# Optimization experiments

Measured on AMD Instinct MI355X. Metric: run time of the kernel, lower is better.

Reference implementation:

```python
import jax, jax.numpy as jnp
import numpy as np

N, C, E, G = 100000, 200, 400000, 512
H, D = 4, 50  # heads, per-head dim (out_channels // num_heads)
NEG_SLOPE = 0.2
EPS_LN = 1e-5


def setup_inputs() -> dict:
    key = jax.random.key(0)
    ks = jax.random.split(key, 12)
    x = jax.random.normal(ks[0], (N, C), dtype=jnp.float32)
    edge_index = jax.random.randint(ks[1], (2, E), 0, N, dtype=jnp.int64)
    batch = jnp.sort(jax.random.randint(ks[2], (N,), 0, G, dtype=jnp.int64))
    # LayerNorm (graph mode) affine params
    ln_w = jnp.ones((C,), jnp.float32)
    ln_b = jnp.zeros((C,), jnp.float32)
    # GATConv params: W [C, H*D], att_src/att_dst [H, D], bias [H*D]
    s = 1.0 / np.sqrt(C)
    W_gat = jax.random.uniform(ks[3], (C, H * D), jnp.float32, -s, s)
    att_src = jax.random.uniform(ks[4], (H, D), jnp.float32, -s, s)
    att_dst = jax.random.uniform(ks[5], (H, D), jnp.float32, -s, s)
    bias_gat = jnp.zeros((H * D,), jnp.float32)
    # SAGPooling scoring GraphConv(C -> 1): lin_rel (with bias) + lin_root (no bias)
    w_rel = jax.random.uniform(ks[6], (C, 1), jnp.float32, -s, s)
    b_rel = jnp.zeros((1,), jnp.float32)
    w_root = jax.random.uniform(ks[7], (C, 1), jnp.float32, -s, s)
    return {"x": x, "edge_index": edge_index, "batch": batch,
            "ln_w": ln_w, "ln_b": ln_b, "W_gat": W_gat, "att_src": att_src,
            "att_dst": att_dst, "bias_gat": bias_gat,
            "w_rel": w_rel, "b_rel": b_rel, "w_root": w_root}


def reference(x, edge_index, batch, ln_w, ln_b, W_gat, att_src, att_dst,
              bias_gat, w_rel, b_rel, w_root):
    n = x.shape[0]
    # --- PyG LayerNorm, mode='graph': normalize over all nodes+channels per graph
    cnt = jax.ops.segment_sum(jnp.ones((n,), x.dtype), batch, G)          # [G]
    denom = cnt * C
    mean = jax.ops.segment_sum(x.sum(-1), batch, G) / denom               # [G]
    ex2 = jax.ops.segment_sum((x * x).sum(-1), batch, G) / denom          # [G]
    var = ex2 - mean * mean
    h = (x - mean[batch, None]) * jax.lax.rsqrt(var + EPS_LN)[batch, None]
    h = h * ln_w + ln_b
    h = jax.nn.elu(h)
    # --- GATConv (concat heads, self-loops added, eval-mode dropout)
    loops = jnp.arange(n, dtype=edge_index.dtype)
    src = jnp.concatenate([edge_index[0], loops])                          # [E+N]
    dst = jnp.concatenate([edge_index[1], loops])
    xh = (h @ W_gat).reshape(n, H, D)                                      # [N,H,D]
    a_src = (xh * att_src).sum(-1)                                         # [N,H]
    a_dst = (xh * att_dst).sum(-1)
    alpha = jax.nn.leaky_relu(a_src[src] + a_dst[dst], NEG_SLOPE)          # [E+N,H]
    m = jax.ops.segment_max(alpha, dst, n)                                 # segment softmax
    e = jnp.exp(alpha - m[dst])
    z = jax.ops.segment_sum(e, dst, n)
    att = e / (z[dst] + 1e-16)
    out = jax.ops.segment_sum(xh[src] * att[:, :, None], dst, n)           # [N,H,D]
    out = out.reshape(n, H * D) + bias_gat                                 # [N,C]
    # --- SAGPooling(min_score=-1): GraphConv score -> per-graph softmax -> multiply
    agg = jax.ops.segment_sum(out[edge_index[0]], edge_index[1], n)        # neighbor sum
    score = (agg @ w_rel + b_rel + out @ w_root)[:, 0]                     # [N]
    sm = score - jax.ops.segment_max(score, batch, G)[batch]
    es = jnp.exp(sm)
    score = es / jax.ops.segment_sum(es, batch, G)[batch]
    # softmax scores in (0,1) > min_score=-1 -> all nodes kept, x scaled by score
    xp = out * score[:, None]                                              # [N,C]
    # --- global_add_pool
    g = jax.ops.segment_sum(xp, batch, G)                                  # [G,C]
    return (xp, g)
```

## Files before the change

### kernel.cpp

```cpp
#include <hip/hip_runtime.h>
#include <hip/hip_bf16.h>

#define NN 100000
#define CC 200
#define EE 400000
#define GG 512

typedef __bf16 bf16x8 __attribute__((ext_vector_type(8)));
typedef float f32x4 __attribute__((ext_vector_type(4)));

__device__ __forceinline__ float bfraw(unsigned int u) { return __uint_as_float(u << 16); }
__device__ __forceinline__ unsigned short f2bfraw(float f) {
  __hip_bfloat16 b = __float2bfloat16(f);
  union { __hip_bfloat16 b; unsigned short u; } cv; cv.b = b; return cv.u;
}

__global__ void k_detect(const unsigned int* __restrict__ lnw_raw,
                         const unsigned int* __restrict__ ei_raw, int* __restrict__ flags) {
  if (threadIdx.x == 0 && blockIdx.x == 0) {
    flags[0] = (lnw_raw[0] == 0x3F800000u) ? 1 : 0;
    flags[1] = (ei_raw[1] == 0u && ei_raw[3] == 0u && ei_raw[5] == 0u && ei_raw[7] == 0u) ? 1 : 0;
  }
}

__global__ void k_cvt_idx(const int* __restrict__ raw, const int* __restrict__ flags,
                          int* __restrict__ out, int count) {
  int i = blockIdx.x * 256 + threadIdx.x;
  if (i >= count) return;
  out[i] = flags[1] ? raw[2 * i] : raw[i];
}

__global__ void k_cvt_params(const void* lnw, const void* lnb, const void* W,
                             const void* attS, const void* attD, const void* bias,
                             const void* wrel, const void* brel, const void* wroot,
                             const int* __restrict__ flags, unsigned short* __restrict__ out) {
  int i = blockIdx.x * 256 + threadIdx.x;
  if (i > 41400) return;
  const void* p; int off;
  if (i < 200)        { p = lnw;  off = i; }
  else if (i < 400)   { p = lnb;  off = i - 200; }
  else if (i < 40400) { p = W;    off = i - 400; }
  else if (i < 40600) { p = attS; off = i - 40400; }
  else if (i < 40800) { p = attD; off = i - 40600; }
  else if (i < 41000) { p = bias; off = i - 40800; }
  else if (i < 41200) { p = wrel; off = i - 41000; }
  else if (i < 41400) { p = wroot; off = i - 41200; }
  else                { p = brel; off = 0; }
  out[i] = flags[0] ? f2bfraw(((const float*)p)[off]) : ((const unsigned short*)p)[off];
}

__global__ void k_starts(const int* __restrict__ batch, int* __restrict__ starts) {
  int i = blockIdx.x * 256 + threadIdx.x;
  if (i >= NN) return;
  int b = batch[i];
  int pb = (i == 0) ? -1 : batch[i - 1];
  for (int g = pb + 1; g <= b; ++g) starts[g] = i;
  if (i == NN - 1) {
    for (int g = b + 1; g <= GG; ++g) starts[g] = NN;
  }
}

__global__ void k_ln_stats(const void* __restrict__ x, const int* __restrict__ starts,
                           const int* __restrict__ flags, float* __restrict__ gacc) {
  __shared__ float sh1[4], sh2[4];
  int g = blockIdx.x >> 3, chunk = blockIdx.x & 7;
  int r0 = starts[g], r1 = starts[g + 1], cnt = r1 - r0;
  int ra = r0 + (cnt * chunk) / 8;
  int rb = r0 + (cnt * (chunk + 1)) / 8;
  float s1 = 0.f, s2 = 0.f;
  if (flags[0]) {
    const float4* xv = (const float4*)x;
    for (int i = ra * 50 + (int)threadIdx.x; i < rb * 50; i += 256) {
      float4 r = xv[i];
      s1 += r.x + r.y + r.z + r.w;
      s2 += r.x * r.x + r.y * r.y + r.z * r.z + r.w * r.w;
    }
  } else {
    const uint4* xv = (const uint4*)x;
    for (int i = ra * 25 + (int)threadIdx.x; i < rb * 25; i += 256) {
      uint4 r = xv[i];
      unsigned int w[4] = {r.x, r.y, r.z, r.w};
#pragma unroll
      for (int j = 0; j < 4; ++j) {
        float a = bfraw(w[j] & 0xffffu);
        float b = bfraw(w[j] >> 16);
        s1 += a + b; s2 += a * a + b * b;
      }
    }
  }
#pragma unroll
  for (int o = 32; o > 0; o >>= 1) { s1 += __shfl_down(s1, o, 64); s2 += __shfl_down(s2, o, 64); }
  if ((threadIdx.x & 63) == 0) { sh1[threadIdx.x >> 6] = s1; sh2[threadIdx.x >> 6] = s2; }
  __syncthreads();
  if (threadIdx.x == 0) {
    atomicAdd(&gacc[g * 2],     sh1[0] + sh1[1] + sh1[2] + sh1[3]);
    atomicAdd(&gacc[g * 2 + 1], sh2[0] + sh2[1] + sh2[2] + sh2[3]);
  }
}

__global__ void k_ln_fin(const float* __restrict__ gacc, const int* __restrict__ starts,
                         float* __restrict__ mean, float* __restrict__ rstd) {
  int g = blockIdx.x * 64 + threadIdx.x;
  if (g >= GG) return;
  int cnt = starts[g + 1] - starts[g];
  if (cnt > 0) {
    float denom = (float)cnt * (float)CC;
    float m = gacc[g * 2] / denom;
    float var = gacc[g * 2 + 1] / denom - m * m;
    mean[g] = m;
    rstd[g] = rsqrtf(var + 1e-5f);
  } else { mean[g] = 0.f; rstd[g] = 0.f; }
}

__global__ void k_norm(const void* __restrict__ x, const int* __restrict__ batch,
                       const float* __restrict__ mean, const float* __restrict__ rstd,
                       const unsigned short* __restrict__ lnw, const unsigned short* __restrict__ lnb,
                       const int* __restrict__ flags, unsigned short* __restrict__ h) {
  int gi = blockIdx.x * 256 + threadIdx.x;
  if (gi >= NN * 25) return;
  int row = gi / 25, sub = gi - row * 25;
  int b = batch[row];
  float m = mean[b], rs = rstd[b];
  int cbase = sub * 8;
  float v[8];
  if (flags[0]) {
    const float* xf = (const float*)x + row * CC + cbase;
    float4 r0 = *(const float4*)xf, r1 = *(const float4*)(xf + 4);
    v[0]=r0.x; v[1]=r0.y; v[2]=r0.z; v[3]=r0.w; v[4]=r1.x; v[5]=r1.y; v[6]=r1.z; v[7]=r1.w;
  } else {
    uint4 r = *(const uint4*)((const unsigned short*)x + row * CC + cbase);
    unsigned int w[4] = {r.x, r.y, r.z, r.w};
#pragma unroll
    for (int j = 0; j < 4; ++j) { v[2*j] = bfraw(w[j] & 0xffffu); v[2*j+1] = bfraw(w[j] >> 16); }
  }
  unsigned int o[4];
#pragma unroll
  for (int j = 0; j < 4; ++j) {
    int c0 = cbase + 2 * j;
    float ta = (v[2*j]   - m) * rs * bfraw(lnw[c0])     + bfraw(lnb[c0]);
    float tb = (v[2*j+1] - m) * rs * bfraw(lnw[c0 + 1]) + bfraw(lnb[c0 + 1]);
    ta = ta > 0.f ? ta : expm1f(ta);
    tb = tb > 0.f ? tb : expm1f(tb);
    o[j] = (unsigned int)f2bfraw(ta) | ((unsigned int)f2bfraw(tb) << 16);
  }
  *(uint4*)(h + row * CC + cbase) = make_uint4(o[0], o[1], o[2], o[3]);
}

__global__ void k_wpack(const unsigned short* __restrict__ W, unsigned short* __restrict__ wp) {
  int idx = blockIdx.x * 256 + threadIdx.x;
  if (idx >= 13 * 7 * 64 * 8) return;
  int j = idx & 7;
  int rest = idx >> 3;
  int l = rest & 63;
  int ts = rest >> 6;
  int s = ts % 7, t = ts / 7;
  int k = s * 32 + (l >> 4) * 8 + j;
  int n = t * 16 + (l & 15);
  wp[idx] = (k < CC && n < CC) ? W[k * CC + n] : (unsigned short)0;
}

__global__ void k_gemm(const unsigned short* __restrict__ h, const unsigned short* __restrict__ wp,
                       unsigned short* __restrict__ xh) {
  int gw = (blockIdx.x * 256 + threadIdx.x) >> 6;
  int lane = threadIdx.x & 63;
  int mbase = gw * 16;
  if (mbase >= NN) return;
  int quad = lane >> 4, l15 = lane & 15;
  f32x4 acc[13];
#pragma unroll
  for (int t = 0; t < 13; ++t) { f32x4 z = {0.f, 0.f, 0.f, 0.f}; acc[t] = z; }
  const unsigned short* hrow = h + (mbase + l15) * CC + quad * 8;
  const bf16x8* wv = (const bf16x8*)wp;
#pragma unroll
  for (int s = 0; s < 7; ++s) {
    bf16x8 af = *(const bf16x8*)(hrow + s * 32);
#pragma unroll
    for (int t = 0; t < 13; ++t) {
      bf16x8 bf = wv[(t * 7 + s) * 64 + lane];
      acc[t] = __builtin_amdgcn_mfma_f32_16x16x32_bf16(af, bf, acc[t], 0, 0, 0);
    }
  }
#pragma unroll
  for (int t = 0; t < 13; ++t) {
    int c = t * 16 + l15;
    if (c < CC) {
#pragma unroll
      for (int r = 0; r < 4; ++r) {
        int mrow = mbase + quad * 4 + r;
        xh[mrow * CC + c] = f2bfraw(acc[t][r]);
      }
    }
  }
}

__global__ void k_attdots(const unsigned short* __restrict__ xh, const unsigned short* __restrict__ attS,
                          const unsigned short* __restrict__ attD,
                          float* __restrict__ asrc, float* __restrict__ adst) {
  int idx = blockIdx.x * 256 + threadIdx.x;
  if (idx >= NN * 4) return;
  int n = idx >> 2, hh = idx & 3;
  const unsigned int* row = (const unsigned int*)(xh + n * CC + hh * 50);
  const unsigned int* ws  = (const unsigned int*)(attS + hh * 50);
  const unsigned int* wd  = (const unsigned int*)(attD + hh * 50);
  float s = 0.f, d = 0.f;
#pragma unroll
  for (int i = 0; i < 25; ++i) {
    unsigned int rv = row[i], sv = ws[i], dv = wd[i];
    float a0 = bfraw(rv & 0xffffu), a1 = bfraw(rv >> 16);
    s += a0 * bfraw(sv & 0xffffu) + a1 * bfraw(sv >> 16);
    d += a0 * bfraw(dv & 0xffffu) + a1 * bfraw(dv >> 16);
  }
  asrc[idx] = s; adst[idx] = d;
}

__global__ void k_hist(const int* __restrict__ ei32, int* __restrict__ deg) {
  int e = blockIdx.x * 256 + threadIdx.x;
  if (e >= EE) return;
  atomicAdd(&deg[ei32[EE + e]], 1);
}

__global__ void k_scan1(const int* __restrict__ deg, int* __restrict__ rowptr, int* __restrict__ sums) {
  __shared__ int sh[256];
  int tid = threadIdx.x;
  int base = blockIdx.x * 1024 + tid * 4;
  int v[4]; int s = 0;
#pragma unroll
  for (int j = 0; j < 4; ++j) { int i = base + j; v[j] = (i < NN) ? deg[i] : 0; s += v[j]; }
  sh[tid] = s;
  __syncthreads();
  for (int o = 1; o < 256; o <<= 1) {
    int t = (tid >= o) ? sh[tid - o] : 0;
    __syncthreads();
    sh[tid] += t;
    __syncthreads();
  }
  int run = sh[tid] - s;
#pragma unroll
  for (int j = 0; j < 4; ++j) { int i = base + j; if (i < NN) rowptr[i] = run; run += v[j]; }
  if (tid == 255) sums[blockIdx.x] = sh[255];
}

__global__ void k_scan2(int* __restrict__ sums, int nb) {
  if (blockIdx.x == 0 && threadIdx.x == 0) {
    int run = 0;
    for (int i = 0; i < nb; ++i) { int t = sums[i]; sums[i] = run; run += t; }
  }
}

__global__ void k_scan3(int* __restrict__ rowptr, const int* __restrict__ sums) {
  int tid = threadIdx.x;
  int add = sums[blockIdx.x];
  int base = blockIdx.x * 1024 + tid * 4;
#pragma unroll
  for (int j = 0; j < 4; ++j) { int i = base + j; if (i < NN) rowptr[i] += add; }
  if (blockIdx.x == 0 && tid == 0) rowptr[NN] = EE;
}

__global__ void k_scatter(const int* __restrict__ ei32, const int* __restrict__ rowptr,
                          int* __restrict__ fill, int* __restrict__ csrc) {
  int e = blockIdx.x * 256 + threadIdx.x;
  if (e >= EE) return;
  int s = ei32[e], d = ei32[EE + e];
  int pos = rowptr[d] + atomicAdd(&fill[d], 1);
  csrc[pos] = s;
}

__global__ void k_attn_z(const float* __restrict__ asrc, const float* __restrict__ adst,
                         const int* __restrict__ rowptr, const int* __restrict__ csrc,
                         float* __restrict__ att, float* __restrict__ z, float* __restrict__ eself) {
  int n = blockIdx.x * 256 + threadIdx.x;
  if (n >= NN) return;
  float4 ad4 = *(const float4*)(adst + n * 4);
  float4 as4 = *(const float4*)(asrc + n * 4);
  float ade[4] = {ad4.x, ad4.y, ad4.z, ad4.w};
  float ase[4] = {as4.x, as4.y, as4.z, as4.w};
  float zz[4], es[4];
#pragma unroll
  for (int hh = 0; hh < 4; ++hh) {
    float al = ase[hh] + ade[hh];
    al = al > 0.f ? al : 0.2f * al;
    es[hh] = __expf(al); zz[hh] = es[hh];
  }
  *(float4*)(eself + n * 4) = make_float4(es[0], es[1], es[2], es[3]);
  int p0 = rowptr[n], p1 = rowptr[n + 1];
  for (int p = p0; p < p1; ++p) {
    int s = csrc[p];
    float4 av = *(const float4*)(asrc + s * 4);
    float a4[4] = {av.x, av.y, av.z, av.w}, e4[4];
#pragma unroll
    for (int hh = 0; hh < 4; ++hh) {
      float al = a4[hh] + ade[hh];
      al = al > 0.f ? al : 0.2f * al;
      e4[hh] = __expf(al);
      zz[hh] += e4[hh];
    }
    *(float4*)(att + p * 4) = make_float4(e4[0], e4[1], e4[2], e4[3]);
  }
  *(float4*)(z + n * 4) = make_float4(zz[0], zz[1], zz[2], zz[3]);
}

__global__ void k_out(const unsigned short* __restrict__ xh, const float* __restrict__ att,
                      const float* __restrict__ z, const float* __restrict__ eself,
                      const int* __restrict__ rowptr, const int* __restrict__ csrc,
                      const unsigned short* __restrict__ bias, const unsigned short* __restrict__ wrel,
                      const unsigned short* __restrict__ wroot,
                      unsigned short* __restrict__ out,
                      float* __restrict__ srel, float* __restrict__ sroot) {
  __shared__ float sA[256], sB[256];
  int tid = threadIdx.x;
  int local = tid / 25;
  int sub = tid - local * 25;
  int n = blockIdx.x * 10 + local;
  bool active = (local < 10) && (n < NN);
  float pr = 0.f, pq = 0.f;
  if (active) {
    int c0 = sub * 8;
    int hh0 = c0 / 50;
    int hh1 = hh0 < 3 ? hh0 + 1 : hh0;
    int bnd = (hh0 + 1) * 50;
    bool cr[8];
#pragma unroll
    for (int j = 0; j < 8; ++j) cr[j] = (c0 + j) >= bnd;
    float e_lo = eself[n * 4 + hh0], e_hi = eself[n * 4 + hh1];
    float rz_lo = 1.f / (z[n * 4 + hh0] + 1e-16f);
    float rz_hi = 1.f / (z[n * 4 + hh1] + 1e-16f);
    float acc[8];
    uint4 xv = *(const uint4*)(xh + (size_t)n * CC + c0);
    {
      unsigned int w[4] = {xv.x, xv.y, xv.z, xv.w};
#pragma unroll
      for (int j = 0; j < 4; ++j) {
        float lo = bfraw(w[j] & 0xffffu), hi = bfraw(w[j] >> 16);
        acc[2*j]   = (cr[2*j]   ? e_hi : e_lo) * lo;
        acc[2*j+1] = (cr[2*j+1] ? e_hi : e_lo) * hi;
      }
    }
    int p0 = rowptr[n], p1 = rowptr[n + 1];
    for (int p = p0; p < p1; ++p) {
      int s = csrc[p];
      float a_lo = att[p * 4 + hh0];
      float a_hi = att[p * 4 + hh1];
      uint4 gv = *(const uint4*)(xh + (size_t)s * CC + c0);
      unsigned int gw[4] = {gv.x, gv.y, gv.z, gv.w};
#pragma unroll
      for (int j = 0; j < 4; ++j) {
        float lo = bfraw(gw[j] & 0xffffu), hi = bfraw(gw[j] >> 16);
        acc[2*j]   += (cr[2*j]   ? a_hi : a_lo) * lo;
        acc[2*j+1] += (cr[2*j+1] ? a_hi : a_lo) * hi;
      }
    }
    uint4 bv = *(const uint4*)(bias + c0);
    uint4 rv = *(const uint4*)(wrel + c0);
    uint4 qv = *(const uint4*)(wroot + c0);
    unsigned int bw[4] = {bv.x, bv.y, bv.z, bv.w};
    unsigned int rw[4] = {rv.x, rv.y, rv.z, rv.w};
    unsigned int qw[4] = {qv.x, qv.y, qv.z, qv.w};
    unsigned int ow[4];
#pragma unroll
    for (int j = 0; j < 4; ++j) {
      float v0 = acc[2*j]   * (cr[2*j]   ? rz_hi : rz_lo) + bfraw(bw[j] & 0xffffu);
      float v1 = acc[2*j+1] * (cr[2*j+1] ? rz_hi : rz_lo) + bfraw(bw[j] >> 16);
      ow[j] = (unsigned int)f2bfraw(v0) | ((unsigned int)f2bfraw(v1) << 16);
      pr += v0 * bfraw(rw[j] & 0xffffu) + v1 * bfraw(rw[j] >> 16);
      pq += v0 * bfraw(qw[j] & 0xffffu) + v1 * bfraw(qw[j] >> 16);
    }
    *(uint4*)(out + (size_t)n * CC + c0) = make_uint4(ow[0], ow[1], ow[2], ow[3]);
  }
  sA[tid] = pr; sB[tid] = pq;
  __syncthreads();
  if (active && sub == 0) {
    float a = 0.f, b = 0.f;
#pragma unroll
    for (int k = 0; k < 25; ++k) { a += sA[tid + k]; b += sB[tid + k]; }
    srel[n] = a; sroot[n] = b;
  }
}

__global__ void k_score(const float* __restrict__ srel, const float* __restrict__ sroot,
                        const unsigned short* __restrict__ brel, const int* __restrict__ rowptr,
                        const int* __restrict__ csrc, float* __restrict__ score) {
  int n = blockIdx.x * 256 + threadIdx.x;
  if (n >= NN) return;
  float sc = bfraw(brel[0]) + sroot[n];
  int p0 = rowptr[n], p1 = rowptr[n + 1];
  for (int p = p0; p < p1; ++p) sc += srel[csrc[p]];
  score[n] = sc;
}

__global__ void k_gsoftmax(const float* __restrict__ score, const int* __restrict__ starts,
                           float* __restrict__ smax, float* __restrict__ ssum) {
  __shared__ float sh[4];
  __shared__ float bc;
  int g = blockIdx.x;
  int r0 = starts[g], r1 = starts[g + 1];
  float m = -3.0e38f;
  for (int i = r0 + (int)threadIdx.x; i < r1; i += 256) m = fmaxf(m, score[i]);
#pragma unroll
  for (int o = 32; o > 0; o >>= 1) m = fmaxf(m, __shfl_down(m, o, 64));
  if ((threadIdx.x & 63) == 0) sh[threadIdx.x >> 6] = m;
  __syncthreads();
  if (threadIdx.x == 0) bc = fmaxf(fmaxf(sh[0], sh[1]), fmaxf(sh[2], sh[3]));
  __syncthreads();
  float mm = bc;
  float s = 0.f;
  for (int i = r0 + (int)threadIdx.x; i < r1; i += 256) s += expf(score[i] - mm);
#pragma unroll
  for (int o = 32; o > 0; o >>= 1) s += __shfl_down(s, o, 64);
  if ((threadIdx.x & 63) == 0) sh[threadIdx.x >> 6] = s;
  __syncthreads();
  if (threadIdx.x == 0) { smax[g] = mm; ssum[g] = sh[0] + sh[1] + sh[2] + sh[3]; }
}

__global__ void k_scoref(const float* __restrict__ score, const int* __restrict__ batch,
                         const float* __restrict__ smax, const float* __restrict__ ssum,
                         float* __restrict__ scoref) {
  int n = blockIdx.x * 256 + threadIdx.x;
  if (n >= NN) return;
  int b = batch[n];
  float d = ssum[b];
  scoref[n] = (d > 0.f) ? expf(score[n] - smax[b]) / d : 0.f;
}

__global__ void k_xp(const unsigned short* __restrict__ out, const float* __restrict__ scoref,
                     const int* __restrict__ flags, void* __restrict__ dout) {
  int gi = blockIdx.x * 256 + threadIdx.x;
  if (gi >= NN * 25) return;
  int r = gi / 25, sub = gi - r * 25;
  float sf = scoref[r];
  uint4 xv = *(const uint4*)(out + (size_t)r * CC + sub * 8);
  unsigned int w[4] = {xv.x, xv.y, xv.z, xv.w};
  if (flags[0]) {
    float v[8];
#pragma unroll
    for (int j = 0; j < 4; ++j) { v[2*j] = bfraw(w[j] & 0xffffu) * sf; v[2*j+1] = bfraw(w[j] >> 16) * sf; }
    float* dp = (float*)dout + (size_t)r * CC + sub * 8;
    *(float4*)dp       = make_float4(v[0], v[1], v[2], v[3]);
    *(float4*)(dp + 4) = make_float4(v[4], v[5], v[6], v[7]);
  } else {
    unsigned int o[4];
#pragma unroll
    for (int j = 0; j < 4; ++j) {
      float lo = bfraw(w[j] & 0xffffu) * sf, hi = bfraw(w[j] >> 16) * sf;
      o[j] = (unsigned int)f2bfraw(lo) | ((unsigned int)f2bfraw(hi) << 16);
    }
    *(uint4*)((unsigned short*)dout + (size_t)r * CC + sub * 8) = make_uint4(o[0], o[1], o[2], o[3]);
  }
}

__global__ void k_gsum(const unsigned short* __restrict__ out, const float* __restrict__ scoref,
                       const int* __restrict__ starts, const int* __restrict__ flags,
                       void* __restrict__ dout) {
  __shared__ float part[10][200];
  int tid = threadIdx.x;
  int rg = tid / 25, sub = tid - rg * 25;
  int g = blockIdx.x;
  int r0 = starts[g], r1 = starts[g + 1];
  if (rg < 10) {
    float acc[8];
#pragma unroll
    for (int j = 0; j < 8; ++j) acc[j] = 0.f;
    for (int r = r0 + rg; r < r1; r += 10) {
      float sf = scoref[r];
      uint4 xv = *(const uint4*)(out + (size_t)r * CC + sub * 8);
      unsigned int w[4] = {xv.x, xv.y, xv.z, xv.w};
#pragma unroll
      for (int j = 0; j < 4; ++j) {
        acc[2*j]   += bfraw(w[j] & 0xffffu) * sf;
        acc[2*j+1] += bfraw(w[j] >> 16) * sf;
      }
    }
#pragma unroll
    for (int j = 0; j < 8; ++j) part[rg][sub * 8 + j] = acc[j];
  }
  __syncthreads();
  if (tid < 200) {
    float s = 0.f;
#pragma unroll
    for (int k = 0; k < 10; ++k) s += part[k][tid];
    size_t o = (size_t)NN * CC + (size_t)g * CC + tid;
    if (flags[0]) ((float*)dout)[o] = s;
    else ((unsigned short*)dout)[o] = f2bfraw(s);
  }
}

constexpr size_t O_FLAGS  = 0;
constexpr size_t O_STARTS = 16;
constexpr size_t O_MEAN   = 2080;
constexpr size_t O_RSTD   = 4128;
constexpr size_t O_SMAX   = 6176;
constexpr size_t O_SSUM   = 8224;
constexpr size_t O_SUMS   = 10272;
constexpr size_t O_PAR    = 10784;
constexpr size_t O_WPACK  = 93600;
constexpr size_t O_BATCH  = 186784;
constexpr size_t O_EI32   = 586784;
constexpr size_t O_DEG    = 3786784;
constexpr size_t O_FILL   = 4186784;
constexpr size_t O_ROWPTR = 4586784;
constexpr size_t O_CSRC   = 4986912;
constexpr size_t O_ASRC   = 6586912;
constexpr size_t O_ADST   = 8186912;
constexpr size_t O_SREL   = 9786912;
constexpr size_t O_SROOT  = 10186912;
constexpr size_t O_SCORE  = 10586912;
constexpr size_t O_SCOREF = 10986912;
constexpr size_t O_Z      = 11386912;
constexpr size_t O_ESELF  = 12986912;
constexpr size_t O_ATT    = 14586912;
constexpr size_t O_XH     = 20986912;
constexpr size_t O_OUT    = 60986912;

extern "C" void kernel_launch(void* const* d_in, const int* in_sizes, int n_in,
                              void* d_out, int out_size, void* d_ws, size_t ws_size,
                              hipStream_t stream) {
  const void* x     = d_in[0];
  const int*  ei    = (const int*)d_in[1];
  const int*  batchr= (const int*)d_in[2];
  const void* lnw_r = d_in[3];
  const void* lnb_r = d_in[4];
  const void* Wg_r  = d_in[5];
  const void* attS_r= d_in[6];
  const void* attD_r= d_in[7];
  const void* bias_r= d_in[8];
  const void* wrel_r= d_in[9];
  const void* brel_r= d_in[10];
  const void* wroot_r=d_in[11];

  char* ws = (char*)d_ws;
  int*   flags  = (int*)(ws + O_FLAGS);
  int*   starts = (int*)(ws + O_STARTS);
  float* mean   = (float*)(ws + O_MEAN);
  float* rstd   = (float*)(ws + O_RSTD);
  float* smax   = (float*)(ws + O_SMAX);
  float* ssum   = (float*)(ws + O_SSUM);
  int*   sums   = (int*)(ws + O_SUMS);
  unsigned short* par = (unsigned short*)(ws + O_PAR);
  unsigned short* wpack = (unsigned short*)(ws + O_WPACK);
  int*   batch  = (int*)(ws + O_BATCH);
  int*   ei32   = (int*)(ws + O_EI32);
  int*   deg    = (int*)(ws + O_DEG);
  int*   fill   = (int*)(ws + O_FILL);
  int*   rowptr = (int*)(ws + O_ROWPTR);
  int*   csrc   = (int*)(ws + O_CSRC);
  float* asrc   = (float*)(ws + O_ASRC);
  float* adst   = (float*)(ws + O_ADST);
  float* srel   = (float*)(ws + O_SREL);
  float* sroot  = (float*)(ws + O_SROOT);
  float* score  = (float*)(ws + O_SCORE);
  float* scoref = (float*)(ws + O_SCOREF);
  float* z      = (float*)(ws + O_Z);
  float* eself  = (float*)(ws + O_ESELF);
  float* att    = (float*)(ws + O_ATT);
  float* gacc   = (float*)(ws + O_ATT);
  unsigned short* xh    = (unsigned short*)(ws + O_XH);
  unsigned short* outws = (unsigned short*)(ws + O_OUT);

  unsigned short* lnw  = par;
  unsigned short* lnb  = par + 200;
  unsigned short* Wc   = par + 400;
  unsigned short* attS = par + 40400;
  unsigned short* attD = par + 40600;
  unsigned short* bias = par + 40800;
  unsigned short* wrel = par + 41000;
  unsigned short* wroot= par + 41200;
  unsigned short* brel = par + 41400;

  unsigned short* h = (unsigned short*)d_out;

  hipMemsetAsync(deg, 0, 800000, stream);
  hipMemsetAsync(gacc, 0, 4096, stream);

  k_detect    <<<1, 64, 0, stream>>>((const unsigned int*)lnw_r, (const unsigned int*)ei, flags);
  k_cvt_params<<<162, 256, 0, stream>>>(lnw_r, lnb_r, Wg_r, attS_r, attD_r, bias_r,
                                        wrel_r, brel_r, wroot_r, flags, par);
  k_cvt_idx   <<<(2 * EE + 255) / 256, 256, 0, stream>>>(ei, flags, ei32, 2 * EE);
  k_cvt_idx   <<<(NN + 255) / 256, 256, 0, stream>>>(batchr, flags, batch, NN);
  k_starts    <<<(NN + 255) / 256, 256, 0, stream>>>(batch, starts);
  k_ln_stats  <<<GG * 8, 256, 0, stream>>>(x, starts, flags, gacc);
  k_ln_fin    <<<8, 64, 0, stream>>>(gacc, starts, mean, rstd);
  k_norm      <<<(NN * 25 + 255) / 256, 256, 0, stream>>>(x, batch, mean, rstd, lnw, lnb, flags, h);
  k_wpack     <<<(13 * 7 * 64 * 8 + 255) / 256, 256, 0, stream>>>(Wc, wpack);
  k_gemm      <<<1563, 256, 0, stream>>>(h, wpack, xh);
  k_attdots   <<<(NN * 4 + 255) / 256, 256, 0, stream>>>(xh, attS, attD, asrc, adst);
  k_hist      <<<(EE + 255) / 256, 256, 0, stream>>>(ei32, deg);
  k_scan1     <<<98, 256, 0, stream>>>(deg, rowptr, sums);
  k_scan2     <<<1, 64, 0, stream>>>(sums, 98);
  k_scan3     <<<98, 256, 0, stream>>>(rowptr, sums);
  k_scatter   <<<(EE + 255) / 256, 256, 0, stream>>>(ei32, rowptr, fill, csrc);
  k_attn_z    <<<(NN + 255) / 256, 256, 0, stream>>>(asrc, adst, rowptr, csrc, att, z, eself);
  k_out       <<<10000, 256, 0, stream>>>(xh, att, z, eself, rowptr, csrc, bias, wrel, wroot,
                                          outws, srel, sroot);
  k_score     <<<(NN + 255) / 256, 256, 0, stream>>>(srel, sroot, brel, rowptr, csrc, score);
  k_gsoftmax  <<<GG, 256, 0, stream>>>(score, starts, smax, ssum);
  k_scoref    <<<(NN + 255) / 256, 256, 0, stream>>>(score, batch, smax, ssum, scoref);
  k_xp        <<<(NN * 25 + 255) / 256, 256, 0, stream>>>(outws, scoref, flags, d_out);
  k_gsum      <<<GG, 256, 0, stream>>>(outws, scoref, starts, flags, d_out);
}
```

Before: 415.6 us.

## Fuse layernorm into GEMM, histogram into edge conversion, and xp with pooling

Layer-norm and ELU are now applied while loading GEMM A fragments, eliminating the intermediate normalized buffer. The degree histogram is folded into edge index conversion, and the block-sum scan becomes a parallel shared-memory scan. The gather loops in the attention-output and score kernels are unrolled by two for more memory-level parallelism. Output scaling and global add pooling are merged into one pass split across 8 chunks per graph, using atomics and a final conversion kernel.

```diff
diff --git a/kernel.cpp b/kernel.cpp
--- a/kernel.cpp
+++ b/kernel.cpp
@@ -28,6 +28,15 @@
   int i = blockIdx.x * 256 + threadIdx.x;
   if (i >= count) return;
   out[i] = flags[1] ? raw[2 * i] : raw[i];
+}
+
+__global__ void k_cvt_edges(const int* __restrict__ raw, const int* __restrict__ flags,
+                            int* __restrict__ out, int* __restrict__ deg) {
+  int i = blockIdx.x * 256 + threadIdx.x;
+  if (i >= 2 * EE) return;
+  int v = flags[1] ? raw[2 * i] : raw[i];
+  out[i] = v;
+  if (i >= EE) atomicAdd(&deg[v], 1);
 }
 
 __global__ void k_cvt_params(const void* lnw, const void* lnb, const void* W,
@@ -112,40 +121,6 @@
   } else { mean[g] = 0.f; rstd[g] = 0.f; }
 }
 
-__global__ void k_norm(const void* __restrict__ x, const int* __restrict__ batch,
-                       const float* __restrict__ mean, const float* __restrict__ rstd,
-                       const unsigned short* __restrict__ lnw, const unsigned short* __restrict__ lnb,
-                       const int* __restrict__ flags, unsigned short* __restrict__ h) {
-  int gi = blockIdx.x * 256 + threadIdx.x;
-  if (gi >= NN * 25) return;
-  int row = gi / 25, sub = gi - row * 25;
-  int b = batch[row];
-  float m = mean[b], rs = rstd[b];
-  int cbase = sub * 8;
-  float v[8];
-  if (flags[0]) {
-    const float* xf = (const float*)x + row * CC + cbase;
-    float4 r0 = *(const float4*)xf, r1 = *(const float4*)(xf + 4);
-    v[0]=r0.x; v[1]=r0.y; v[2]=r0.z; v[3]=r0.w; v[4]=r1.x; v[5]=r1.y; v[6]=r1.z; v[7]=r1.w;
-  } else {
-    uint4 r = *(const uint4*)((const unsigned short*)x + row * CC + cbase);
-    unsigned int w[4] = {r.x, r.y, r.z, r.w};
-#pragma unroll
-    for (int j = 0; j < 4; ++j) { v[2*j] = bfraw(w[j] & 0xffffu); v[2*j+1] = bfraw(w[j] >> 16); }
-  }
-  unsigned int o[4];
-#pragma unroll
-  for (int j = 0; j < 4; ++j) {
-    int c0 = cbase + 2 * j;
-    float ta = (v[2*j]   - m) * rs * bfraw(lnw[c0])     + bfraw(lnb[c0]);
-    float tb = (v[2*j+1] - m) * rs * bfraw(lnw[c0 + 1]) + bfraw(lnb[c0 + 1]);
-    ta = ta > 0.f ? ta : expm1f(ta);
-    tb = tb > 0.f ? tb : expm1f(tb);
-    o[j] = (unsigned int)f2bfraw(ta) | ((unsigned int)f2bfraw(tb) << 16);
-  }
-  *(uint4*)(h + row * CC + cbase) = make_uint4(o[0], o[1], o[2], o[3]);
-}
-
 __global__ void k_wpack(const unsigned short* __restrict__ W, unsigned short* __restrict__ wp) {
   int idx = blockIdx.x * 256 + threadIdx.x;
   if (idx >= 13 * 7 * 64 * 8) return;
@@ -159,25 +134,61 @@
   wp[idx] = (k < CC && n < CC) ? W[k * CC + n] : (unsigned short)0;
 }
 
-__global__ void k_gemm(const unsigned short* __restrict__ h, const unsigned short* __restrict__ wp,
-                       unsigned short* __restrict__ xh) {
+__global__ void k_ngemm(const void* __restrict__ x, const int* __restrict__ batch,
+                        const float* __restrict__ mean, const float* __restrict__ rstd,
+                        const unsigned short* __restrict__ lnw, const unsigned short* __restrict__ lnb,
+                        const unsigned short* __restrict__ wp, const int* __restrict__ flags,
+                        unsigned short* __restrict__ xh) {
   int gw = (blockIdx.x * 256 + threadIdx.x) >> 6;
   int lane = threadIdx.x & 63;
   int mbase = gw * 16;
   if (mbase >= NN) return;
   int quad = lane >> 4, l15 = lane & 15;
+  int row = mbase + l15;
+  int b = batch[row];
+  float m = mean[b], rs = rstd[b];
+  bool f32in = flags[0] != 0;
   f32x4 acc[13];
 #pragma unroll
-  for (int t = 0; t < 13; ++t) { f32x4 z = {0.f, 0.f, 0.f, 0.f}; acc[t] = z; }
-  const unsigned short* hrow = h + (mbase + l15) * CC + quad * 8;
+  for (int t = 0; t < 13; ++t) { f32x4 zz = {0.f, 0.f, 0.f, 0.f}; acc[t] = zz; }
   const bf16x8* wv = (const bf16x8*)wp;
 #pragma unroll
   for (int s = 0; s < 7; ++s) {
-    bf16x8 af = *(const bf16x8*)(hrow + s * 32);
+    int kb = s * 32 + quad * 8;
+    union { bf16x8 v; unsigned short u[8]; unsigned int w[4]; } af;
+    if (kb < CC) {
+      float v[8];
+      if (f32in) {
+        const float* xp = (const float*)x + (size_t)row * CC + kb;
+        float4 a = *(const float4*)xp, c = *(const float4*)(xp + 4);
+        v[0]=a.x; v[1]=a.y; v[2]=a.z; v[3]=a.w; v[4]=c.x; v[5]=c.y; v[6]=c.z; v[7]=c.w;
+      } else {
+        uint4 r = *(const uint4*)((const unsigned short*)x + (size_t)row * CC + kb);
+        unsigned int w[4] = {r.x, r.y, r.z, r.w};
+#pragma unroll
+        for (int j = 0; j < 4; ++j) { v[2*j] = bfraw(w[j] & 0xffffu); v[2*j+1] = bfraw(w[j] >> 16); }
+      }
+      uint4 wv4 = *(const uint4*)(lnw + kb);
+      uint4 bv4 = *(const uint4*)(lnb + kb);
+      unsigned int ww[4] = {wv4.x, wv4.y, wv4.z, wv4.w};
+      unsigned int bb[4] = {bv4.x, bv4.y, bv4.z, bv4.w};
+#pragma unroll
+      for (int j = 0; j < 4; ++j) {
+        float t0 = (v[2*j]   - m) * rs * bfraw(ww[j] & 0xffffu) + bfraw(bb[j] & 0xffffu);
+        float t1 = (v[2*j+1] - m) * rs * bfraw(ww[j] >> 16)     + bfraw(bb[j] >> 16);
+        t0 = t0 > 0.f ? t0 : __expf(t0) - 1.f;
+        t1 = t1 > 0.f ? t1 : __expf(t1) - 1.f;
+        af.u[2*j]   = f2bfraw(t0);
+        af.u[2*j+1] = f2bfraw(t1);
+      }
+    } else {
+#pragma unroll
+      for (int j = 0; j < 4; ++j) af.w[j] = 0u;
+    }
 #pragma unroll
     for (int t = 0; t < 13; ++t) {
       bf16x8 bf = wv[(t * 7 + s) * 64 + lane];
-      acc[t] = __builtin_amdgcn_mfma_f32_16x16x32_bf16(af, bf, acc[t], 0, 0, 0);
+      acc[t] = __builtin_amdgcn_mfma_f32_16x16x32_bf16(af.v, bf, acc[t], 0, 0, 0);
     }
   }
 #pragma unroll
@@ -187,7 +198,7 @@
 #pragma unroll
       for (int r = 0; r < 4; ++r) {
         int mrow = mbase + quad * 4 + r;
-        xh[mrow * CC + c] = f2bfraw(acc[t][r]);
+        xh[(size_t)mrow * CC + c] = f2bfraw(acc[t][r]);
       }
     }
   }
@@ -199,7 +210,7 @@
   int idx = blockIdx.x * 256 + threadIdx.x;
   if (idx >= NN * 4) return;
   int n = idx >> 2, hh = idx & 3;
-  const unsigned int* row = (const unsigned int*)(xh + n * CC + hh * 50);
+  const unsigned int* row = (const unsigned int*)(xh + (size_t)n * CC + hh * 50);
   const unsigned int* ws  = (const unsigned int*)(attS + hh * 50);
   const unsigned int* wd  = (const unsigned int*)(attD + hh * 50);
   float s = 0.f, d = 0.f;
@@ -213,12 +224,6 @@
   asrc[idx] = s; adst[idx] = d;
 }
 
-__global__ void k_hist(const int* __restrict__ ei32, int* __restrict__ deg) {
-  int e = blockIdx.x * 256 + threadIdx.x;
-  if (e >= EE) return;
-  atomicAdd(&deg[ei32[EE + e]], 1);
-}
-
 __global__ void k_scan1(const int* __restrict__ deg, int* __restrict__ rowptr, int* __restrict__ sums) {
   __shared__ int sh[256];
   int tid = threadIdx.x;
@@ -241,10 +246,18 @@
 }
 
 __global__ void k_scan2(int* __restrict__ sums, int nb) {
-  if (blockIdx.x == 0 && threadIdx.x == 0) {
-    int run = 0;
-    for (int i = 0; i < nb; ++i) { int t = sums[i]; sums[i] = run; run += t; }
-  }
+  __shared__ int sh[128];
+  int tid = threadIdx.x;
+  int v = (tid < nb) ? sums[tid] : 0;
+  sh[tid] = v;
+  __syncthreads();
+  for (int o = 1; o < 128; o <<= 1) {
+    int t = (tid >= o) ? sh[tid - o] : 0;
+    __syncthreads();
+    sh[tid] += t;
+    __syncthreads();
+  }
+  if (tid < nb) sums[tid] = sh[tid] - v;
 }
 
 __global__ void k_scan3(int* __restrict__ rowptr, const int* __restrict__ sums) {
@@ -270,8 +283,8 @@
                          float* __restrict__ att, float* __restrict__ z, float* __restrict__ eself) {
   int n = blockIdx.x * 256 + threadIdx.x;
   if (n >= NN) return;
-  float4 ad4 = *(const float4*)(adst + n * 4);
-  float4 as4 = *(const float4*)(asrc + n * 4);
+  float4 ad4 = *(const float4*)(adst + (size_t)n * 4);
+  float4 as4 = *(const float4*)(asrc + (size_t)n * 4);
   float ade[4] = {ad4.x, ad4.y, ad4.z, ad4.w};
   float ase[4] = {as4.x, as4.y, as4.z, as4.w};
   float zz[4], es[4];
@@ -281,11 +294,11 @@
     al = al > 0.f ? al : 0.2f * al;
     es[hh] = __expf(al); zz[hh] = es[hh];
   }
-  *(float4*)(eself + n * 4) = make_float4(es[0], es[1], es[2], es[3]);
+  *(float4*)(eself + (size_t)n * 4) = make_float4(es[0], es[1], es[2], es[3]);
   int p0 = rowptr[n], p1 = rowptr[n + 1];
   for (int p = p0; p < p1; ++p) {
     int s = csrc[p];
-    float4 av = *(const float4*)(asrc + s * 4);
+    float4 av = *(const float4*)(asrc + (size_t)s * 4);
     float a4[4] = {av.x, av.y, av.z, av.w}, e4[4];
 #pragma unroll
     for (int hh = 0; hh < 4; ++hh) {
@@ -294,9 +307,9 @@
       e4[hh] = __expf(al);
       zz[hh] += e4[hh];
     }
-    *(float4*)(att + p * 4) = make_float4(e4[0], e4[1], e4[2], e4[3]);
-  }
-  *(float4*)(z + n * 4) = make_float4(zz[0], zz[1], zz[2], zz[3]);
+    *(float4*)(att + (size_t)p * 4) = make_float4(e4[0], e4[1], e4[2], e4[3]);
+  }
+  *(float4*)(z + (size_t)n * 4) = make_float4(zz[0], zz[1], zz[2], zz[3]);
 }
 
 __global__ void k_out(const unsigned short* __restrict__ xh, const float* __restrict__ att,
@@ -325,8 +338,8 @@
     float rz_lo = 1.f / (z[n * 4 + hh0] + 1e-16f);
     float rz_hi = 1.f / (z[n * 4 + hh1] + 1e-16f);
     float acc[8];
-    uint4 xv = *(const uint4*)(xh + (size_t)n * CC + c0);
     {
+      uint4 xv = *(const uint4*)(xh + (size_t)n * CC + c0);
       unsigned int w[4] = {xv.x, xv.y, xv.z, xv.w};
 #pragma unroll
       for (int j = 0; j < 4; ++j) {
@@ -336,17 +349,41 @@
       }
     }
     int p0 = rowptr[n], p1 = rowptr[n + 1];
-    for (int p = p0; p < p1; ++p) {
-      int s = csrc[p];
-      float a_lo = att[p * 4 + hh0];
-      float a_hi = att[p * 4 + hh1];
-      uint4 gv = *(const uint4*)(xh + (size_t)s * CC + c0);
-      unsigned int gw[4] = {gv.x, gv.y, gv.z, gv.w};
+    int p = p0;
+    for (; p + 2 <= p1; p += 2) {
+      int s0 = csrc[p], s1 = csrc[p + 1];
+      uint4 g0 = *(const uint4*)(xh + (size_t)s0 * CC + c0);
+      uint4 g1 = *(const uint4*)(xh + (size_t)s1 * CC + c0);
+      float4 av0 = *(const float4*)(att + (size_t)p * 4);
+      float4 av1 = *(const float4*)(att + (size_t)(p + 1) * 4);
+      float a0lo = hh0 == 0 ? av0.x : hh0 == 1 ? av0.y : hh0 == 2 ? av0.z : av0.w;
+      float a0hi = hh1 == 1 ? av0.y : hh1 == 2 ? av0.z : av0.w;
+      float a1lo = hh0 == 0 ? av1.x : hh0 == 1 ? av1.y : hh0 == 2 ? av1.z : av1.w;
+      float a1hi = hh1 == 1 ? av1.y : hh1 == 2 ? av1.z : av1.w;
+      unsigned int w0[4] = {g0.x, g0.y, g0.z, g0.w};
+      unsigned int w1[4] = {g1.x, g1.y, g1.z, g1.w};
 #pragma unroll
       for (int j = 0; j < 4; ++j) {
-        float lo = bfraw(gw[j] & 0xffffu), hi = bfraw(gw[j] >> 16);
-        acc[2*j]   += (cr[2*j]   ? a_hi : a_lo) * lo;
-        acc[2*j+1] += (cr[2*j+1] ? a_hi : a_lo) * hi;
+        acc[2*j]   += (cr[2*j]   ? a0hi : a0lo) * bfraw(w0[j] & 0xffffu);
+        acc[2*j+1] += (cr[2*j+1] ? a0hi : a0lo) * bfraw(w0[j] >> 16);
+      }
+#pragma unroll
+      for (int j = 0; j < 4; ++j) {
+        acc[2*j]   += (cr[2*j]   ? a1hi : a1lo) * bfraw(w1[j] & 0xffffu);
+        acc[2*j+1] += (cr[2*j+1] ? a1hi : a1lo) * bfraw(w1[j] >> 16);
+      }
+    }
+    if (p < p1) {
+      int s0 = csrc[p];
+      uint4 g0 = *(const uint4*)(xh + (size_t)s0 * CC + c0);
+      float4 av0 = *(const float4*)(att + (size_t)p * 4);
+      float a0lo = hh0 == 0 ? av0.x : hh0 == 1 ? av0.y : hh0 == 2 ? av0.z : av0.w;
+      float a0hi = hh1 == 1 ? av0.y : hh1 == 2 ? av0.z : av0.w;
+      unsigned int w0[4] = {g0.x, g0.y, g0.z, g0.w};
+#pragma unroll
+      for (int j = 0; j < 4; ++j) {
+        acc[2*j]   += (cr[2*j]   ? a0hi : a0lo) * bfraw(w0[j] & 0xffffu);
+        acc[2*j+1] += (cr[2*j+1] ? a0hi : a0lo) * bfraw(w0[j] >> 16);
       }
     }
     uint4 bv = *(const uint4*)(bias + c0);
@@ -383,8 +420,11 @@
   if (n >= NN) return;
   float sc = bfraw(brel[0]) + sroot[n];
   int p0 = rowptr[n], p1 = rowptr[n + 1];
-  for (int p = p0; p < p1; ++p) sc += srel[csrc[p]];
-  score[n] = sc;
+  int p = p0;
+  float s0 = 0.f, s1 = 0.f;
+  for (; p + 2 <= p1; p += 2) { s0 += srel[csrc[p]]; s1 += srel[csrc[p + 1]]; }
+  if (p < p1) s0 += srel[csrc[p]];
+  score[n] = sc + s0 + s1;
 }
 
 __global__ void k_gsoftmax(const float* __restrict__ score, const int* __restrict__ starts,
@@ -421,52 +461,42 @@
   scoref[n] = (d > 0.f) ? expf(score[n] - smax[b]) / d : 0.f;
 }
 
-__global__ void k_xp(const unsigned short* __restrict__ out, const float* __restrict__ scoref,
-                     const int* __restrict__ flags, void* __restrict__ dout) {
-  int gi = blockIdx.x * 256 + threadIdx.x;
-  if (gi >= NN * 25) return;
-  int r = gi / 25, sub = gi - r * 25;
-  float sf = scoref[r];
-  uint4 xv = *(const uint4*)(out + (size_t)r * CC + sub * 8);
-  unsigned int w[4] = {xv.x, xv.y, xv.z, xv.w};
-  if (flags[0]) {
-    float v[8];
-#pragma unroll
-    for (int j = 0; j < 4; ++j) { v[2*j] = bfraw(w[j] & 0xffffu) * sf; v[2*j+1] = bfraw(w[j] >> 16) * sf; }
-    float* dp = (float*)dout + (size_t)r * CC + sub * 8;
-    *(float4*)dp       = make_float4(v[0], v[1], v[2], v[3]);
-    *(float4*)(dp + 4) = make_float4(v[4], v[5], v[6], v[7]);
-  } else {
-    unsigned int o[4];
-#pragma unroll
-    for (int j = 0; j < 4; ++j) {
-      float lo = bfraw(w[j] & 0xffffu) * sf, hi = bfraw(w[j] >> 16) * sf;
-      o[j] = (unsigned int)f2bfraw(lo) | ((unsigned int)f2bfraw(hi) << 16);
-    }
-    *(uint4*)((unsigned short*)dout + (size_t)r * CC + sub * 8) = make_uint4(o[0], o[1], o[2], o[3]);
-  }
-}
-
-__global__ void k_gsum(const unsigned short* __restrict__ out, const float* __restrict__ scoref,
-                       const int* __restrict__ starts, const int* __restrict__ flags,
-                       void* __restrict__ dout) {
+__global__ void k_xpg(const unsigned short* __restrict__ out, const float* __restrict__ scoref,
+                      const int* __restrict__ starts, const int* __restrict__ flags,
+                      void* __restrict__ dout, float* __restrict__ gsum) {
   __shared__ float part[10][200];
+  int g = blockIdx.x >> 3, chunk = blockIdx.x & 7;
+  int r0 = starts[g], r1 = starts[g + 1], cnt = r1 - r0;
+  int ra = r0 + (cnt * chunk) / 8;
+  int rb = r0 + (cnt * (chunk + 1)) / 8;
   int tid = threadIdx.x;
   int rg = tid / 25, sub = tid - rg * 25;
-  int g = blockIdx.x;
-  int r0 = starts[g], r1 = starts[g + 1];
+  int f32o = flags[0];
   if (rg < 10) {
     float acc[8];
 #pragma unroll
     for (int j = 0; j < 8; ++j) acc[j] = 0.f;
-    for (int r = r0 + rg; r < r1; r += 10) {
+    for (int r = ra + rg; r < rb; r += 10) {
       float sf = scoref[r];
       uint4 xv = *(const uint4*)(out + (size_t)r * CC + sub * 8);
       unsigned int w[4] = {xv.x, xv.y, xv.z, xv.w};
+      float v[8];
 #pragma unroll
       for (int j = 0; j < 4; ++j) {
-        acc[2*j]   += bfraw(w[j] & 0xffffu) * sf;
-        acc[2*j+1] += bfraw(w[j] >> 16) * sf;
+        v[2*j]   = bfraw(w[j] & 0xffffu) * sf;
+        v[2*j+1] = bfraw(w[j] >> 16) * sf;
+        acc[2*j] += v[2*j]; acc[2*j+1] += v[2*j+1];
+      }
+      if (f32o) {
+        float* dp = (float*)dout + (size_t)r * CC + sub * 8;
+        *(float4*)dp       = make_float4(v[0], v[1], v[2], v[3]);
+        *(float4*)(dp + 4) = make_float4(v[4], v[5], v[6], v[7]);
+      } else {
+        unsigned int o[4];
+#pragma unroll
+        for (int j = 0; j < 4; ++j)
+          o[j] = (unsigned int)f2bfraw(v[2*j]) | ((unsigned int)f2bfraw(v[2*j+1]) << 16);
+        *(uint4*)((unsigned short*)dout + (size_t)r * CC + sub * 8) = make_uint4(o[0], o[1], o[2], o[3]);
       }
     }
 #pragma unroll
@@ -477,10 +507,18 @@
     float s = 0.f;
 #pragma unroll
     for (int k = 0; k < 10; ++k) s += part[k][tid];
-    size_t o = (size_t)NN * CC + (size_t)g * CC + tid;
-    if (flags[0]) ((float*)dout)[o] = s;
-    else ((unsigned short*)dout)[o] = f2bfraw(s);
-  }
+    atomicAdd(&gsum[g * 200 + tid], s);
+  }
+}
+
+__global__ void k_gfin(const float* __restrict__ gsum, const int* __restrict__ flags,
+                       void* __restrict__ dout) {
+  int i = blockIdx.x * 256 + threadIdx.x;
+  if (i >= GG * 200) return;
+  float s = gsum[i];
+  size_t o = (size_t)NN * CC + i;
+  if (flags[0]) ((float*)dout)[o] = s;
+  else ((unsigned short*)dout)[o] = f2bfraw(s);
 }
 
 constexpr size_t O_FLAGS  = 0;
@@ -552,6 +590,7 @@
   float* eself  = (float*)(ws + O_ESELF);
   float* att    = (float*)(ws + O_ATT);
   float* gacc   = (float*)(ws + O_ATT);
+  float* gsum   = (float*)(ws + O_ATT + 4096);
   unsigned short* xh    = (unsigned short*)(ws + O_XH);
   unsigned short* outws = (unsigned short*)(ws + O_OUT);
 
@@ -565,34 +604,31 @@
   unsigned short* wroot= par + 41200;
   unsigned short* brel = par + 41400;
 
-  unsigned short* h = (unsigned short*)d_out;
-
   hipMemsetAsync(deg, 0, 800000, stream);
   hipMemsetAsync(gacc, 0, 4096, stream);
 
   k_detect    <<<1, 64, 0, stream>>>((const unsigned int*)lnw_r, (const unsigned int*)ei, flags);
   k_cvt_params<<<162, 256, 0, stream>>>(lnw_r, lnb_r, Wg_r, attS_r, attD_r, bias_r,
                                         wrel_r, brel_r, wroot_r, flags, par);
-  k_cvt_idx   <<<(2 * EE + 255) / 256, 256, 0, stream>>>(ei, flags, ei32, 2 * EE);
+  k_cvt_edges <<<(2 * EE + 255) / 256, 256, 0, stream>>>(ei, flags, ei32, deg);
   k_cvt_idx   <<<(NN + 255) / 256, 256, 0, stream>>>(batchr, flags, batch, NN);
   k_starts    <<<(NN + 255) / 256, 256, 0, stream>>>(batch, starts);
   k_ln_stats  <<<GG * 8, 256, 0, stream>>>(x, starts, flags, gacc);
   k_ln_fin    <<<8, 64, 0, stream>>>(gacc, starts, mean, rstd);
-  k_norm      <<<(NN * 25 + 255) / 256, 256, 0, stream>>>(x, batch, mean, rstd, lnw, lnb, flags, h);
   k_wpack     <<<(13 * 7 * 64 * 8 + 255) / 256, 256, 0, stream>>>(Wc, wpack);
-  k_gemm      <<<1563, 256, 0, stream>>>(h, wpack, xh);
+  k_ngemm     <<<1563, 256, 0, stream>>>(x, batch, mean, rstd, lnw, lnb, wpack, flags, xh);
   k_attdots   <<<(NN * 4 + 255) / 256, 256, 0, stream>>>(xh, attS, attD, asrc, adst);
-  k_hist      <<<(EE + 255) / 256, 256, 0, stream>>>(ei32, deg);
   k_scan1     <<<98, 256, 0, stream>>>(deg, rowptr, sums);
-  k_scan2     <<<1, 64, 0, stream>>>(sums, 98);
+  k_scan2     <<<1, 128, 0, stream>>>(sums, 98);
   k_scan3     <<<98, 256, 0, stream>>>(rowptr, sums);
   k_scatter   <<<(EE + 255) / 256, 256, 0, stream>>>(ei32, rowptr, fill, csrc);
   k_attn_z    <<<(NN + 255) / 256, 256, 0, stream>>>(asrc, adst, rowptr, csrc, att, z, eself);
   k_out       <<<10000, 256, 0, stream>>>(xh, att, z, eself, rowptr, csrc, bias, wrel, wroot,
                                           outws, srel, sroot);
+  hipMemsetAsync(gsum, 0, 409600, stream);
   k_score     <<<(NN + 255) / 256, 256, 0, stream>>>(srel, sroot, brel, rowptr, csrc, score);
   k_gsoftmax  <<<GG, 256, 0, stream>>>(score, starts, smax, ssum);
   k_scoref    <<<(NN + 255) / 256, 256, 0, stream>>>(score, batch, smax, ssum, scoref);
-  k_xp        <<<(NN * 25 + 255) / 256, 256, 0, stream>>>(outws, scoref, flags, d_out);
-  k_gsum      <<<GG, 256, 0, stream>>>(outws, scoref, starts, flags, d_out);
-}
+  k_xpg       <<<GG * 8, 256, 0, stream>>>(outws, scoref, starts, flags, d_out, gsum);
+  k_gfin      <<<(GG * 200 + 255) / 256, 256, 0, stream>>>(gsum, flags, d_out);
+}
```

Result: faster. 372.0 us (-10.5%).
